# Kernel optimization log

Hardware: AMD Instinct MI355X
Metric: run time of the kernel (lower is better)

The kernel has to match this reference:

```python
import jax, jax.numpy as jnp
import numpy as np

N_IMG, BATCH, SEQ, D_IN, H = 32, 1024, 64, 16, 16


def setup_inputs() -> dict:
    key = jax.random.key(0)
    k1, k2, k3, k4, k5 = jax.random.split(key, 5)
    s = 1.0 / np.sqrt(H)  # torch nn.LSTM default init: U(-1/sqrt(H), 1/sqrt(H))
    return {
        "images": jax.random.normal(k1, (N_IMG, BATCH, SEQ, D_IN), jnp.float32),
        "w_ih": jax.random.uniform(k2, (4 * H, D_IN), jnp.float32, -s, s),
        "w_hh": jax.random.uniform(k3, (4 * H, H), jnp.float32, -s, s),
        "b_ih": jax.random.uniform(k4, (4 * H,), jnp.float32, -s, s),
        "b_hh": jax.random.uniform(k5, (4 * H,), jnp.float32, -s, s),
    }


def reference(images, w_ih, w_hh, b_ih, b_hh):
    # images: [N, B, S, D]. The torch module loops over N chunks, feeding each
    # [B, S, D] chunk through nn.LSTM while carrying (h, c) across chunks.
    # Equivalent: one continuous recurrence over N*S timesteps.
    n, b, s, d = images.shape
    h_dim = w_hh.shape[1]
    # time-major: [N*S, B, D]
    xs = images.transpose(0, 2, 1, 3).reshape(n * s, b, d)
    # precompute input projections for all timesteps (the only big GEMM)
    x_proj = jnp.einsum('tbd,gd->tbg', xs, w_ih) + (b_ih + b_hh)  # [T, B, 4H]

    def cell(carry, xp_t):
        h_prev, c_prev = carry
        gates = xp_t + h_prev @ w_hh.T  # [B, 4H]; torch gate order: i, f, g, o
        i, f, g, o = jnp.split(gates, 4, axis=-1)
        c = jax.nn.sigmoid(f) * c_prev + jax.nn.sigmoid(i) * jnp.tanh(g)
        h_new = jax.nn.sigmoid(o) * jnp.tanh(c)
        return (h_new, c), h_new

    h0 = jnp.zeros((b, h_dim), images.dtype)
    (_, _), outs = jax.lax.scan(cell, (h0, h0), x_proj)  # outs: [T, B, H]
    # torch stacks per-chunk outputs [B, S, H] along dim 0 -> [N, B, S, H]
    return outs.reshape(n, s, b, h_dim).transpose(0, 2, 1, 3)
```

## Files before the change

### kernel.cpp

```cpp
#include <hip/hip_runtime.h>

#define LOG2E      1.44269504088896340736f
#define TWO_LOG2E  2.88539008177792680472f

typedef float f2 __attribute__((ext_vector_type(2)));

__device__ __forceinline__ float frcp(float x)  { return __builtin_amdgcn_rcpf(x); }
__device__ __forceinline__ float fexp2(float x) { return __builtin_amdgcn_exp2f(x); }

__device__ __forceinline__ f2 pk_mul(f2 a, f2 b) {
    f2 d; asm("v_pk_mul_f32 %0, %1, %2" : "=v"(d) : "v"(a), "v"(b)); return d;
}
__device__ __forceinline__ f2 pk_fma(f2 a, f2 b, f2 c) {
    f2 d; asm("v_pk_fma_f32 %0, %1, %2, %3" : "=v"(d) : "v"(a), "v"(b), "v"(c)); return d;
}
__device__ __forceinline__ f2 pk_add(f2 a, f2 b) {
    f2 d; asm("v_pk_add_f32 %0, %1, %2" : "=v"(d) : "v"(a), "v"(b)); return d;
}
__device__ __forceinline__ f2 f2lo(float4 v) { f2 r; r.x = v.x; r.y = v.y; return r; }
__device__ __forceinline__ f2 f2hi(float4 v) { f2 r; r.x = v.z; r.y = v.w; return r; }

__device__ __forceinline__ void gload_lds16(const float* g, float* l) {
    auto gp = (const __attribute__((address_space(1))) float*)g;
    auto lp = (__attribute__((address_space(3))) float*)l;
    __builtin_amdgcn_global_load_lds(gp, lp, 16, 0, 0);
}


__global__ __launch_bounds__(256, 1)
void lstm_fused(const float* __restrict__ images,
                const float* __restrict__ w_ih,
                const float* __restrict__ w_hh,
                const float* __restrict__ b_ih,
                const float* __restrict__ b_hh,
                float* __restrict__ out)
{
    __shared__ float4 xlds[4][2][256];

    const int lane = threadIdx.x & 63;
    const int wid  = threadIdx.x >> 6;
    const int b    = (blockIdx.x << 2) + wid;
    const int a    = lane >> 4;
    const int j    = lane & 15;

    int rr1 = __builtin_amdgcn_update_dpp(0, j, 0x121, 0xF, 0xF, true);
    const int d_ror = (rr1 - j) & 15;

    int e16;
    { int pa = a, pb = a;
      asm volatile("s_nop 1\n\t"
                   "v_permlane16_swap_b32 %0, %1" : "+v"(pa), "+v"(pb));
      e16 = pa & 1; }
    int e32;
    { int pc = a, pd = a;
      asm volatile("s_nop 1\n\t"
                   "v_permlane32_swap_b32 %0, %1" : "+v"(pc), "+v"(pd));
      e32 = (pc < 2) ? 0 : 1; }

    const int m1 = ((a >> 1) == e32);
    const int m0 = ((a & 1) == e16);
    const int gate = m0 ? (m1 ? 1 : 2) : (m1 ? 0 : 3);
    const int r = gate * 16 + j;

    const float aa = (gate == 2) ? TWO_LOG2E : -LOG2E;
    const float mm = (gate == 2) ? -2.0f * TWO_LOG2E : 1.0f;
    const float dd = (gate == 2) ? TWO_LOG2E : 0.0f;

    float whh[16];
#pragma unroll
    for (int t = 0; t < 16; ++t)
        whh[t] = aa * w_hh[r * 16 + ((j + d_ror * t) & 15)];
    f2 wihp[8];
#pragma unroll
    for (int m = 0; m < 8; ++m) {
        f2 w; w.x = aa * w_ih[r * 16 + 2 * m]; w.y = aa * w_ih[r * 16 + 2 * m + 1];
        wihp[m] = w;
    }
    const float bias = aa * (b_ih[r] + b_hh[r]);

    const bool su0 = (a == 0), su1 = (a == 1), su2 = (a == 2), su3 = (a == 3);

    float hv = 0.0f;
    float c  = 0.0f;
    float sv = 0.0f;

    const int bbase = b << 10;

#define PB(p) ((((p) >> 4) << 20) + bbase + (((((p) << 2)) & 63) << 4))

#define GLOAD_CHUNK(n) {                                                       \
        const float* gp_ = images + ((n) << 20) + bbase + (lane << 2);         \
        float4* lb_ = &xlds[wid][(n) & 1][0];                                  \
        gload_lds16(gp_ + 0,   (float*)(lb_ + 0));                             \
        gload_lds16(gp_ + 256, (float*)(lb_ + 64));                            \
        gload_lds16(gp_ + 512, (float*)(lb_ + 128));                           \
        gload_lds16(gp_ + 768, (float*)(lb_ + 192)); }

#define DSREADV(xv, Qraw) {                                                    \
        int Q_ = (Qraw); if (Q_ > 511) Q_ = 511;                               \
        auto lp_ = (const __attribute__((address_space(3))) float4*)           \
                   &xlds[wid][(Q_ >> 4) & 1][(Q_ & 15) << 4];                  \
        _Pragma("unroll")                                                      \
        for (int q = 0; q < 16; ++q)                                           \
            asm volatile("ds_read_b128 %0, %1 offset:%2"                       \
                : "=v"(xv[q]) : "v"(lp_), "i"(q * 16) : "memory");             \
    }

#define WAIT_LGKM() { asm volatile("s_waitcnt lgkmcnt(0)" ::: "memory");       \
                      __builtin_amdgcn_sched_barrier(0); }

#define PROJ(xpre, xv) {                                                       \
        _Pragma("unroll")                                                      \
        for (int u = 0; u < 4; ++u) {                                          \
            f2 A_ = pk_mul(wihp[0], f2lo(xv[4*u+0]));                          \
            f2 B_ = pk_mul(wihp[1], f2hi(xv[4*u+0]));                          \
            A_ = pk_fma(wihp[2], f2lo(xv[4*u+1]), A_);                         \
            B_ = pk_fma(wihp[3], f2hi(xv[4*u+1]), B_);                         \
            A_ = pk_fma(wihp[4], f2lo(xv[4*u+2]), A_);                         \
            B_ = pk_fma(wihp[5], f2hi(xv[4*u+2]), B_);                         \
            A_ = pk_fma(wihp[6], f2lo(xv[4*u+3]), A_);                         \
            B_ = pk_fma(wihp[7], f2hi(xv[4*u+3]), B_);                         \
            A_ = pk_add(A_, B_);                                               \
            xpre[u] = (bias + A_.x) + A_.y;                                    \
        } }

#define STEP(SU, xpv) {                                                        \
        float p0 = (xpv), p1, p2, p3;                                          \
        asm("s_nop 1\n\t"                                                      \
          "v_fmac_f32 %[q0], %[h], %[w0]\n\t"                                  \
          "v_mul_f32 %[q1], %[h], %[w1] row_ror:1 row_mask:0xf bank_mask:0xf\n\t" \
          "v_mul_f32 %[q2], %[h], %[w2] row_ror:2 row_mask:0xf bank_mask:0xf\n\t" \
          "v_mul_f32 %[q3], %[h], %[w3] row_ror:3 row_mask:0xf bank_mask:0xf\n\t" \
          "v_fmac_f32 %[q0], %[h], %[w4] row_ror:4 row_mask:0xf bank_mask:0xf\n\t" \
          "v_fmac_f32 %[q1], %[h], %[w5] row_ror:5 row_mask:0xf bank_mask:0xf\n\t" \
          "v_fmac_f32 %[q2], %[h], %[w6] row_ror:6 row_mask:0xf bank_mask:0xf\n\t" \
          "v_fmac_f32 %[q3], %[h], %[w7] row_ror:7 row_mask:0xf bank_mask:0xf\n\t" \
          "v_fmac_f32 %[q0], %[h], %[w8] row_ror:8 row_mask:0xf bank_mask:0xf\n\t" \
          "v_fmac_f32 %[q1], %[h], %[w9] row_ror:9 row_mask:0xf bank_mask:0xf\n\t" \
          "v_fmac_f32 %[q2], %[h], %[w10] row_ror:10 row_mask:0xf bank_mask:0xf\n\t" \
          "v_fmac_f32 %[q3], %[h], %[w11] row_ror:11 row_mask:0xf bank_mask:0xf\n\t" \
          "v_fmac_f32 %[q0], %[h], %[w12] row_ror:12 row_mask:0xf bank_mask:0xf\n\t" \
          "v_fmac_f32 %[q1], %[h], %[w13] row_ror:13 row_mask:0xf bank_mask:0xf\n\t" \
          "v_fmac_f32 %[q2], %[h], %[w14] row_ror:14 row_mask:0xf bank_mask:0xf\n\t" \
          "v_fmac_f32 %[q3], %[h], %[w15] row_ror:15 row_mask:0xf bank_mask:0xf"   \
          : [q0]"+v"(p0), [q1]"=&v"(p1), [q2]"=&v"(p2), [q3]"=&v"(p3)          \
          : [h]"v"(hv),                                                        \
            [w0]"v"(whh[0]),  [w1]"v"(whh[1]),  [w2]"v"(whh[2]),  [w3]"v"(whh[3]), \
            [w4]"v"(whh[4]),  [w5]"v"(whh[5]),  [w6]"v"(whh[6]),  [w7]"v"(whh[7]), \
            [w8]"v"(whh[8]),  [w9]"v"(whh[9]),  [w10]"v"(whh[10]),[w11]"v"(whh[11]),\
            [w12]"v"(whh[12]),[w13]"v"(whh[13]),[w14]"v"(whh[14]),[w15]"v"(whh[15]));\
        float arg = (p0 + p1) + (p2 + p3);                                     \
        float act = fmaf(mm, frcp(1.0f + fexp2(arg)), dd);                     \
        float qf, qg, qi, qo;                                                  \
        asm("v_mov_b32 %[A], %[x]\n\t"                                         \
          "v_mov_b32 %[B], %[x]\n\t"                                           \
          "s_nop 1\n\t"                                                        \
          "v_permlane16_swap_b32 %[A], %[B]\n\t"                               \
          "v_mov_b32 %[C], %[A]\n\t"                                           \
          "v_mov_b32 %[D], %[B]\n\t"                                           \
          "v_permlane32_swap_b32 %[A], %[C]\n\t"                               \
          "v_permlane32_swap_b32 %[B], %[D]"                                   \
          : [A]"=&v"(qf), [B]"=&v"(qi), [C]"=&v"(qg), [D]"=&v"(qo)             \
          : [x]"v"(act));                                                      \
        float ig = qi * qg;                                                    \
        float qo2 = qo + qo;                                                   \
        c = fmaf(c, qf, ig);                                                   \
        float rr = frcp(1.0f + fexp2(c));                                      \
        hv = fmaf(-qo2, rr, qo);                                               \
        sv = (SU) ? hv : sv;                                                   \
    }

#define STORE(pb) out[(pb) + lane] = sv;

    float4 xv[16];
    float  xpre[4];

    GLOAD_CHUNK(0);
    GLOAD_CHUNK(1);
    asm volatile("s_waitcnt vmcnt(0)" ::: "memory");
    DSREADV(xv, 0);
    WAIT_LGKM();
    PROJ(xpre, xv);

#pragma unroll 1
    for (int P = 0; P < 512; ++P) {
        DSREADV(xv, P + 1);
        {
            const int pb = PB(P);
            STEP(su0, xpre[0]);
            STEP(su1, xpre[1]);
            STEP(su2, xpre[2]);
            STEP(su3, xpre[3]);
            STORE(pb);
        }
        if ((P & 15) == 8)
            asm volatile("s_waitcnt vmcnt(0)" ::: "memory");
        WAIT_LGKM();
        PROJ(xpre, xv);
        if ((P & 15) == 14 && P < 480)
            GLOAD_CHUNK((P >> 4) + 2);
    }

#undef STEP
#undef STORE
#undef PROJ
#undef WAIT_LGKM
#undef DSREADV
#undef GLOAD_CHUNK
#undef PB
}

extern "C" void kernel_launch(void* const* d_in, const int* in_sizes, int n_in,
                              void* d_out, int out_size, void* d_ws, size_t ws_size,
                              hipStream_t stream)
{
    const float* images = (const float*)d_in[0];
    const float* w_ih   = (const float*)d_in[1];
    const float* w_hh   = (const float*)d_in[2];
    const float* b_ih   = (const float*)d_in[3];
    const float* b_hh   = (const float*)d_in[4];
    float* outp         = (float*)d_out;

    lstm_fused<<<dim3(256), dim3(256), 0, stream>>>(images, w_ih, w_hh, b_ih, b_hh, outp);
}
```

Measured before the change: 317.1 us.

## Load per-step inputs via scalar loads instead of LDS staging

Replaces the global-to-LDS double-buffered staging and per-lane ds_read_b128 of the 16x16 input tile with wave-uniform s_load_dwordx16 scalar loads into SGPRs, one per sub-step row. The input projection becomes scalar-operand FMAs against per-lane W_ih weights, removing the LDS traffic and the vmcnt waits. In exchange each step issues scalar memory loads whose latency must be hidden behind the recurrence, and it uses many SGPRs.

```diff
diff --git a/kernel.cpp b/kernel.cpp
--- a/kernel.cpp
+++ b/kernel.cpp
@@ -3,28 +3,10 @@
 #define LOG2E      1.44269504088896340736f
 #define TWO_LOG2E  2.88539008177792680472f
 
-typedef float f2 __attribute__((ext_vector_type(2)));
+typedef float f16v __attribute__((ext_vector_type(16)));
 
 __device__ __forceinline__ float frcp(float x)  { return __builtin_amdgcn_rcpf(x); }
 __device__ __forceinline__ float fexp2(float x) { return __builtin_amdgcn_exp2f(x); }
-
-__device__ __forceinline__ f2 pk_mul(f2 a, f2 b) {
-    f2 d; asm("v_pk_mul_f32 %0, %1, %2" : "=v"(d) : "v"(a), "v"(b)); return d;
-}
-__device__ __forceinline__ f2 pk_fma(f2 a, f2 b, f2 c) {
-    f2 d; asm("v_pk_fma_f32 %0, %1, %2, %3" : "=v"(d) : "v"(a), "v"(b), "v"(c)); return d;
-}
-__device__ __forceinline__ f2 pk_add(f2 a, f2 b) {
-    f2 d; asm("v_pk_add_f32 %0, %1, %2" : "=v"(d) : "v"(a), "v"(b)); return d;
-}
-__device__ __forceinline__ f2 f2lo(float4 v) { f2 r; r.x = v.x; r.y = v.y; return r; }
-__device__ __forceinline__ f2 f2hi(float4 v) { f2 r; r.x = v.z; r.y = v.w; return r; }
-
-__device__ __forceinline__ void gload_lds16(const float* g, float* l) {
-    auto gp = (const __attribute__((address_space(1))) float*)g;
-    auto lp = (__attribute__((address_space(3))) float*)l;
-    __builtin_amdgcn_global_load_lds(gp, lp, 16, 0, 0);
-}
 
 
 __global__ __launch_bounds__(256, 1)
@@ -35,8 +17,6 @@
                 const float* __restrict__ b_hh,
                 float* __restrict__ out)
 {
-    __shared__ float4 xlds[4][2][256];
-
     const int lane = threadIdx.x & 63;
     const int wid  = threadIdx.x >> 6;
     const int b    = (blockIdx.x << 2) + wid;
@@ -70,12 +50,10 @@
 #pragma unroll
     for (int t = 0; t < 16; ++t)
         whh[t] = aa * w_hh[r * 16 + ((j + d_ror * t) & 15)];
-    f2 wihp[8];
+    float wih[16];
 #pragma unroll
-    for (int m = 0; m < 8; ++m) {
-        f2 w; w.x = aa * w_ih[r * 16 + 2 * m]; w.y = aa * w_ih[r * 16 + 2 * m + 1];
-        wihp[m] = w;
-    }
+    for (int k = 0; k < 16; ++k)
+        wih[k] = aa * w_ih[r * 16 + k];
     const float bias = aa * (b_ih[r] + b_hh[r]);
 
     const bool su0 = (a == 0), su1 = (a == 1), su2 = (a == 2), su3 = (a == 3);
@@ -85,44 +63,42 @@
     float sv = 0.0f;
 
     const int bbase = b << 10;
+    const unsigned wb = __builtin_amdgcn_readfirstlane(b);
+    const unsigned long long img_u = (unsigned long long)images;
 
 #define PB(p) ((((p) >> 4) << 20) + bbase + (((((p) << 2)) & 63) << 4))
 
-#define GLOAD_CHUNK(n) {                                                       \
-        const float* gp_ = images + ((n) << 20) + bbase + (lane << 2);         \
-        float4* lb_ = &xlds[wid][(n) & 1][0];                                  \
-        gload_lds16(gp_ + 0,   (float*)(lb_ + 0));                             \
-        gload_lds16(gp_ + 256, (float*)(lb_ + 64));                            \
-        gload_lds16(gp_ + 512, (float*)(lb_ + 128));                           \
-        gload_lds16(gp_ + 768, (float*)(lb_ + 192)); }
+#define SBASE(p) (img_u + (((unsigned long long)((p) >> 4)) << 22)             \
+                        + (((unsigned long long)wb) << 12)                     \
+                        + (unsigned long long)(((p) & 15) << 8))
 
-#define DSREADV(xv, Qraw) {                                                    \
+#define SLOADP(Qraw) {                                                         \
         int Q_ = (Qraw); if (Q_ > 511) Q_ = 511;                               \
-        auto lp_ = (const __attribute__((address_space(3))) float4*)           \
-                   &xlds[wid][(Q_ >> 4) & 1][(Q_ & 15) << 4];                  \
-        _Pragma("unroll")                                                      \
-        for (int q = 0; q < 16; ++q)                                           \
-            asm volatile("ds_read_b128 %0, %1 offset:%2"                       \
-                : "=v"(xv[q]) : "v"(lp_), "i"(q * 16) : "memory");             \
+        unsigned long long sb_ = SBASE(Q_);                                    \
+        asm volatile("s_load_dwordx16 %0, %4, 0x0\n\t"                         \
+                     "s_load_dwordx16 %1, %4, 0x40\n\t"                        \
+                     "s_load_dwordx16 %2, %4, 0x80\n\t"                        \
+                     "s_load_dwordx16 %3, %4, 0xc0"                            \
+                     : "=s"(sx0), "=s"(sx1), "=s"(sx2), "=s"(sx3)              \
+                     : "s"(sb_));                                              \
     }
 
 #define WAIT_LGKM() { asm volatile("s_waitcnt lgkmcnt(0)" ::: "memory");       \
                       __builtin_amdgcn_sched_barrier(0); }
 
-#define PROJ(xpre, xv) {                                                       \
+#define PROJ1(dst, sx) {                                                       \
+        float s0_ = bias, s1_ = 0.f, s2_ = 0.f, s3_ = 0.f;                     \
         _Pragma("unroll")                                                      \
-        for (int u = 0; u < 4; ++u) {                                          \
-            f2 A_ = pk_mul(wihp[0], f2lo(xv[4*u+0]));                          \
-            f2 B_ = pk_mul(wihp[1], f2hi(xv[4*u+0]));                          \
-            A_ = pk_fma(wihp[2], f2lo(xv[4*u+1]), A_);                         \
-            B_ = pk_fma(wihp[3], f2hi(xv[4*u+1]), B_);                         \
-            A_ = pk_fma(wihp[4], f2lo(xv[4*u+2]), A_);                         \
-            B_ = pk_fma(wihp[5], f2hi(xv[4*u+2]), B_);                         \
-            A_ = pk_fma(wihp[6], f2lo(xv[4*u+3]), A_);                         \
-            B_ = pk_fma(wihp[7], f2hi(xv[4*u+3]), B_);                         \
-            A_ = pk_add(A_, B_);                                               \
-            xpre[u] = (bias + A_.x) + A_.y;                                    \
-        } }
+        for (int k_ = 0; k_ < 4; ++k_) {                                       \
+            s0_ = fmaf(sx[4*k_+0], wih[4*k_+0], s0_);                          \
+            s1_ = fmaf(sx[4*k_+1], wih[4*k_+1], s1_);                          \
+            s2_ = fmaf(sx[4*k_+2], wih[4*k_+2], s2_);                          \
+            s3_ = fmaf(sx[4*k_+3], wih[4*k_+3], s3_);                          \
+        }                                                                      \
+        dst = (s0_ + s1_) + (s2_ + s3_);                                       \
+    }
+#define PROJ4() { PROJ1(xpre[0], sx0); PROJ1(xpre[1], sx1);                    \
+                  PROJ1(xpre[2], sx2); PROJ1(xpre[3], sx3); }
 
 #define STEP(SU, xpv) {                                                        \
         float p0 = (xpv), p1, p2, p3;                                          \
@@ -172,19 +148,16 @@
 
 #define STORE(pb) out[(pb) + lane] = sv;
 
-    float4 xv[16];
-    float  xpre[4];
+    f16v  sx0, sx1, sx2, sx3;
+    float xpre[4];
 
-    GLOAD_CHUNK(0);
-    GLOAD_CHUNK(1);
-    asm volatile("s_waitcnt vmcnt(0)" ::: "memory");
-    DSREADV(xv, 0);
+    SLOADP(0);
     WAIT_LGKM();
-    PROJ(xpre, xv);
+    PROJ4();
 
 #pragma unroll 1
     for (int P = 0; P < 512; ++P) {
-        DSREADV(xv, P + 1);
+        SLOADP(P + 1);
         {
             const int pb = PB(P);
             STEP(su0, xpre[0]);
@@ -193,20 +166,17 @@
             STEP(su3, xpre[3]);
             STORE(pb);
         }
-        if ((P & 15) == 8)
-            asm volatile("s_waitcnt vmcnt(0)" ::: "memory");
         WAIT_LGKM();
-        PROJ(xpre, xv);
-        if ((P & 15) == 14 && P < 480)
-            GLOAD_CHUNK((P >> 4) + 2);
+        PROJ4();
     }
 
 #undef STEP
 #undef STORE
-#undef PROJ
+#undef PROJ4
+#undef PROJ1
 #undef WAIT_LGKM
-#undef DSREADV
-#undef GLOAD_CHUNK
+#undef SLOADP
+#undef SBASE
 #undef PB
 }
 
```

New measurement: 311.3 us. No clear change (-1.8%).
